# Performance work log

Measured on AMD Instinct MI355X. Metric: run time of the kernel, lower is better.

## Reference

```python
import jax, jax.numpy as jnp
import numpy as np
from jax import lax

B, C, H, W = 32, 256, 64, 64
MCH = 16   # max(8, 256//16)
KS = 5     # ECA 1D kernel: int((log2(256)+1)/2)=4 -> odd-adjust 5
EPS = 1e-5

def setup_inputs() -> dict:
    key = jax.random.key(0)
    ks = jax.random.split(key, 9)
    return {
        "x": jax.random.normal(ks[0], (B, C, H, W), jnp.float32),
        "w10": jax.random.normal(ks[1], (MCH, C), jnp.float32) * 0.05,   # 1x1 conv C->MCH
        "w11": jax.random.normal(ks[2], (C, MCH), jnp.float32) * 0.05,   # 1x1 conv MCH->C
        "bn_gamma": jax.random.normal(ks[3], (MCH,), jnp.float32) * 0.1 + 1.0,
        "bn_beta": jax.random.normal(ks[4], (MCH,), jnp.float32) * 0.1,
        "bn_mean": jax.random.normal(ks[5], (MCH,), jnp.float32) * 0.1,
        "bn_var": jax.random.uniform(ks[6], (MCH,), jnp.float32, 0.5, 1.5),
        "w20": jax.random.normal(ks[7], (KS,), jnp.float32) * 0.2,       # 1D ECA kernel
        "w21": jax.random.normal(ks[8], (1, 1, 3, 3), jnp.float32) * 0.2,  # spatial 3x3
    }

def reference(x, w10, w11, bn_gamma, bn_beta, bn_mean, bn_var, w20, w21):
    b, c, h, w = x.shape
    # --- channel (ECA) branch: global avg pool -> 1D conv over channel dim ---
    pooled = jnp.mean(x, axis=(2, 3))                      # [b, c]
    f_ch = lax.conv_general_dilated(
        pooled[:, None, :], w20[None, None, :], (1,), 'SAME',
        dimension_numbers=('NCH', 'OIH', 'NCH'))[:, 0, :]   # [b, c]
    f_ch = f_ch[:, :, None, None]                           # [b, c, 1, 1] (no sigmoid, as in source)
    # --- spatial branch: channel mean -> 3x3 conv -> sigmoid ---
    f_sa = jax.nn.sigmoid(lax.conv_general_dilated(
        jnp.mean(x, axis=1, keepdims=True), w21, (1, 1), 'SAME',
        dimension_numbers=('NCHW', 'OIHW', 'NCHW')))        # [b, 1, h, w]
    # --- coordinate branch ---
    x_h = jnp.mean(x, axis=3)                               # [b, c, h]
    x_w = jnp.mean(x, axis=2)                               # [b, c, w]
    cat = jnp.concatenate([x_h, x_w], axis=2)               # [b, c, h+w]
    y = jnp.einsum('mc,bcl->bml', w10, cat)                 # 1x1 conv
    inv = lax.rsqrt(bn_var + EPS) * bn_gamma                # BN (inference)
    y = jax.nn.relu(y * inv[None, :, None] + (bn_beta - bn_mean * inv)[None, :, None])
    yh, yw = y[:, :, :h], y[:, :, h:]
    s_h = jax.nn.sigmoid(jnp.einsum('cm,bmh->bch', w11, yh))[:, :, :, None]  # [b,c,h,1]
    s_w = jax.nn.sigmoid(jnp.einsum('cm,bmw->bcw', w11, yw))[:, :, None, :]  # [b,c,1,w]
    F = f_ch + s_h * s_w + f_sa
    return x * F
```

## Files before the change

### kernel.cpp

```cpp
#include <hip/hip_runtime.h>
#include <hip/hip_bf16.h>

#define NB 32
#define NC 256
#define NH 64
#define NW 64

typedef unsigned short u16;

__device__ int   g_mode;
__device__ float g_cmeanp[NB * 16 * 4096];
__device__ float g_catT[NB * 128 * NC];
__device__ float g_fch[NB * NC];
__device__ float g_fsa[NB * 4096];
__device__ float g_sh[NB * NC * 64];
__device__ float g_sw[NB * NC * 64];

__device__ __forceinline__ float bf2f(unsigned int u) {
    union { unsigned int i; float f; } v; v.i = u << 16; return v.f;
}
__device__ __forceinline__ u16 f2bf(float f) {
    union { float f; unsigned int i; } v; v.f = f;
    unsigned int i = v.i;
    unsigned int r = (i + 0x7fffu + ((i >> 16) & 1u)) >> 16;
    return (u16)r;
}
__device__ __forceinline__ unsigned int pack2(float a, float b) {
    return (unsigned int)f2bf(a) | ((unsigned int)f2bf(b) << 16);
}
__device__ __forceinline__ float sigmoidf_(float x) {
    return 1.f / (1.f + expf(-x));
}

__device__ __forceinline__ void loadx8(const void* x, size_t i8, int mode, float* v) {
    if (mode) {
        const uint4 u = ((const uint4*)x)[i8];
        v[0] = bf2f(u.x & 0xffffu); v[1] = bf2f(u.x >> 16);
        v[2] = bf2f(u.y & 0xffffu); v[3] = bf2f(u.y >> 16);
        v[4] = bf2f(u.z & 0xffffu); v[5] = bf2f(u.z >> 16);
        v[6] = bf2f(u.w & 0xffffu); v[7] = bf2f(u.w >> 16);
    } else {
        const float4 a = ((const float4*)x)[i8 * 2];
        const float4 b = ((const float4*)x)[i8 * 2 + 1];
        v[0] = a.x; v[1] = a.y; v[2] = a.z; v[3] = a.w;
        v[4] = b.x; v[5] = b.y; v[6] = b.z; v[7] = b.w;
    }
}
__device__ __forceinline__ float loadw(const void* p, int i, int mode) {
    return mode ? bf2f((unsigned int)((const u16*)p)[i]) : ((const float*)p)[i];
}
__device__ __forceinline__ void store8(void* o, size_t i8, int mode, const float* v) {
    if (mode) {
        uint4 u;
        u.x = pack2(v[0], v[1]);
        u.y = pack2(v[2], v[3]);
        u.z = pack2(v[4], v[5]);
        u.w = pack2(v[6], v[7]);
        ((uint4*)o)[i8] = u;
    } else {
        ((float4*)o)[i8 * 2]     = make_float4(v[0], v[1], v[2], v[3]);
        ((float4*)o)[i8 * 2 + 1] = make_float4(v[4], v[5], v[6], v[7]);
    }
}

__global__ __launch_bounds__(256) void kSniff(const u16* __restrict__ xr) {
    __shared__ int cnt;
    if (threadIdx.x == 0) cnt = 0;
    __syncthreads();
    int local = 0;
#pragma unroll
    for (int i = 0; i < 8; ++i) {
        const u16 w = xr[(threadIdx.x * 8 + i) * 2];
        const unsigned e = (w >> 7) & 0xffu;
        if (w == 0 || (e >= 0x40u && e <= 0x90u)) ++local;
    }
    atomicAdd(&cnt, local);
    __syncthreads();
    if (threadIdx.x == 0) g_mode = (cnt >= 1536) ? 1 : 0;
}

__global__ __launch_bounds__(256) void kA(const void* __restrict__ x) {
    __shared__ unsigned int sliceP[4][2048];
    __shared__ float rowsum[16 * 64];
    __shared__ float colsum[16 * 64];

    const int t  = threadIdx.x;
    const int ln = t & 63, wv = t >> 6;
    const int cg = blockIdx.x;
    const int b  = blockIdx.y;
    const int mode = g_mode;

    float colacc[4][8];
#pragma unroll
    for (int cc = 0; cc < 4; ++cc)
#pragma unroll
        for (int k = 0; k < 8; ++k) colacc[cc][k] = 0.f;

    const int ch0 = cg * 16 + wv * 4;
    const size_t i8base = (((size_t)(b * NC + ch0)) << 9) + ln;

    for (int p = 0; p < 8; ++p) {
        float cme[8];
#pragma unroll
        for (int k = 0; k < 8; ++k) cme[k] = 0.f;
#pragma unroll
        for (int cc = 0; cc < 4; ++cc) {
            float v[8];
            loadx8(x, i8base + (((size_t)cc) << 9) + p * 64, mode, v);
#pragma unroll
            for (int k = 0; k < 8; ++k) {
                cme[k] += v[k];
                colacc[cc][k] += v[k];
            }
            float s = ((v[0] + v[1]) + (v[2] + v[3])) + ((v[4] + v[5]) + (v[6] + v[7]));
            s += __shfl_xor(s, 1);
            s += __shfl_xor(s, 2);
            s += __shfl_xor(s, 4);
            if ((ln & 7) == 0)
                rowsum[(wv * 4 + cc) * 64 + p * 8 + (ln >> 3)] = s;
        }
        uint4 pk;
        pk.x = pack2(cme[0], cme[1]);
        pk.y = pack2(cme[2], cme[3]);
        pk.z = pack2(cme[4], cme[5]);
        pk.w = pack2(cme[6], cme[7]);
        *(uint4*)&sliceP[wv][p * 256 + ln * 4] = pk;
    }

#pragma unroll
    for (int cc = 0; cc < 4; ++cc)
#pragma unroll
        for (int k = 0; k < 8; ++k) {
            float v = colacc[cc][k];
            v += __shfl_xor(v, 8);
            v += __shfl_xor(v, 16);
            v += __shfl_xor(v, 32);
            colacc[cc][k] = v;
        }
    if (ln < 8) {
#pragma unroll
        for (int cc = 0; cc < 4; ++cc) {
            *(float4*)&colsum[(wv * 4 + cc) * 64 + ln * 8] =
                make_float4(colacc[cc][0], colacc[cc][1], colacc[cc][2], colacc[cc][3]);
            *(float4*)&colsum[(wv * 4 + cc) * 64 + ln * 8 + 4] =
                make_float4(colacc[cc][4], colacc[cc][5], colacc[cc][6], colacc[cc][7]);
        }
    }
    __syncthreads();

    const float inv64 = 1.f / 64.f;
    {
        const int lc = t & 15;
#pragma unroll
        for (int r = 0; r < 8; ++r) {
            const int l = r * 16 + (t >> 4);
            const float val =
                (l < 64 ? rowsum[lc * 64 + l] : colsum[lc * 64 + (l - 64)]) * inv64;
            g_catT[((size_t)(b * 128 + l)) * NC + cg * 16 + lc] = val;
        }
    }
    {
        const int u0 = t * 8;
        float acc[16];
#pragma unroll
        for (int k = 0; k < 16; ++k) acc[k] = 0.f;
#pragma unroll
        for (int w = 0; w < 4; ++w) {
            const uint4 qa = *(const uint4*)&sliceP[w][u0];
            const uint4 qb = *(const uint4*)&sliceP[w][u0 + 4];
            const unsigned int uu[8] = {qa.x, qa.y, qa.z, qa.w, qb.x, qb.y, qb.z, qb.w};
#pragma unroll
            for (int k = 0; k < 8; ++k) {
                acc[2 * k]     += bf2f(uu[k] & 0xffffu);
                acc[2 * k + 1] += bf2f(uu[k] >> 16);
            }
        }
        const float invC = 1.f / 256.f;
        float* dst = g_cmeanp + (((size_t)(b * 16 + cg)) << 12) + t * 16;
#pragma unroll
        for (int k4 = 0; k4 < 4; ++k4)
            *(float4*)(dst + k4 * 4) = make_float4(acc[k4 * 4] * invC,
                                                   acc[k4 * 4 + 1] * invC,
                                                   acc[k4 * 4 + 2] * invC,
                                                   acc[k4 * 4 + 3] * invC);
    }
}

__global__ __launch_bounds__(256) void kB(
    const void* __restrict__ w10, const void* __restrict__ w11,
    const void* __restrict__ bn_gamma, const void* __restrict__ bn_beta,
    const void* __restrict__ bn_mean, const void* __restrict__ bn_var,
    const void* __restrict__ w20, const void* __restrict__ w21) {

    __shared__ float w10_lds[16 * 260];
    __shared__ float w11_lds[2048];
    __shared__ float y_lds[16 * 65];
    __shared__ float cm[4096];
    __shared__ float pooled[260];
    __shared__ float bnA[16], bnBv[16];

    const int t  = threadIdx.x;
    const int bx = blockIdx.x;
    const int half = bx >> 1, csplit = bx & 1;
    const int b  = blockIdx.y;
    const int mode = g_mode;

    for (int j = t; j < 4096; j += 256)
        w10_lds[(j >> 8) * 260 + (j & 255)] = loadw(w10, j, mode);
    for (int j = t; j < 2048; j += 256)
        w11_lds[j] = loadw(w11, csplit * 2048 + j, mode);
    if (t < 16) {
        const float inv = rsqrtf(loadw(bn_var, t, mode) + 1e-5f) *
                          loadw(bn_gamma, t, mode);
        bnA[t]  = inv;
        bnBv[t] = loadw(bn_beta, t, mode) - loadw(bn_mean, t, mode) * inv;
    }
    __syncthreads();

    {
        const int m = t & 15, li = t >> 4;
#pragma unroll
        for (int rep = 0; rep < 4; ++rep) {
            const int l = rep * 16 + li;
            const float4* cr =
                (const float4*)(g_catT + ((size_t)(b * 128 + half * 64 + l)) * NC);
            const float4* wr = (const float4*)(w10_lds + m * 260);
            float acc = 0.f;
#pragma unroll 8
            for (int c4 = 0; c4 < 64; ++c4) {
                const float4 a = wr[c4], v = cr[c4];
                acc = fmaf(a.x, v.x, fmaf(a.y, v.y, fmaf(a.z, v.z, fmaf(a.w, v.w, acc))));
            }
            y_lds[m * 65 + l] = fmaxf(fmaf(acc, bnA[m], bnBv[m]), 0.f);
        }
    }
    __syncthreads();

    {
        const int h = t & 63, q = t >> 6;
        float yr[16];
#pragma unroll
        for (int mm = 0; mm < 16; ++mm) yr[mm] = y_lds[mm * 65 + h];
        float* sout = half ? g_sw : g_sh;
        const size_t sb = ((size_t)b) * NC * 64;
        for (int ci = 0; ci < 32; ++ci) {
            const int cl = q * 32 + ci;
            const float4* wrow = (const float4*)(w11_lds + cl * 16);
            const float4 w0 = wrow[0], w1 = wrow[1], w2 = wrow[2], w3 = wrow[3];
            float acc;
            acc = fmaf(w0.x, yr[0], w0.y * yr[1]);
            acc = fmaf(w0.z, yr[2], acc); acc = fmaf(w0.w, yr[3], acc);
            acc = fmaf(w1.x, yr[4], acc); acc = fmaf(w1.y, yr[5], acc);
            acc = fmaf(w1.z, yr[6], acc); acc = fmaf(w1.w, yr[7], acc);
            acc = fmaf(w2.x, yr[8], acc); acc = fmaf(w2.y, yr[9], acc);
            acc = fmaf(w2.z, yr[10], acc); acc = fmaf(w2.w, yr[11], acc);
            acc = fmaf(w3.x, yr[12], acc); acc = fmaf(w3.y, yr[13], acc);
            acc = fmaf(w3.z, yr[14], acc); acc = fmaf(w3.w, yr[15], acc);
            sout[sb + (size_t)(csplit * 128 + cl) * 64 + h] = sigmoidf_(acc);
        }
    }

    if (bx == 0) {
        float p = 0.f;
        for (int l = 0; l < 64; ++l)
            p += g_catT[((size_t)(b * 128 + l)) * NC + t];
        pooled[2 + t] = p * (1.f / 64.f);
        if (t < 2) { pooled[t] = 0.f; pooled[258 + t] = 0.f; }
        __syncthreads();
        float w20f[5];
#pragma unroll
        for (int k = 0; k < 5; ++k) w20f[k] = loadw(w20, k, mode);
        float acc = 0.f;
#pragma unroll
        for (int k = 0; k < 5; ++k) acc = fmaf(w20f[k], pooled[t + k], acc);
        g_fch[b * NC + t] = acc;
    } else if (bx == 1) {
#pragma unroll
        for (int it = 0; it < 4; ++it) {
            const int j = it * 1024 + t * 4;
            float4 s = make_float4(0.f, 0.f, 0.f, 0.f);
            for (int gcg = 0; gcg < 16; ++gcg) {
                const float4 v =
                    *(const float4*)&g_cmeanp[(((size_t)(b * 16 + gcg)) << 12) + j];
                s.x += v.x; s.y += v.y; s.z += v.z; s.w += v.w;
            }
            *(float4*)&cm[j] = s;
        }
        __syncthreads();
        float w21f[9];
#pragma unroll
        for (int k = 0; k < 9; ++k) w21f[k] = loadw(w21, k, mode);
        for (int r = 0; r < 16; ++r) {
            const int j = r * 256 + t;
            const int hh = j >> 6, ww = j & 63;
            float acc = 0.f;
#pragma unroll
            for (int dy = 0; dy < 3; ++dy) {
                const int hy = hh + dy - 1;
                if (hy < 0 || hy > 63) continue;
#pragma unroll
                for (int dx = 0; dx < 3; ++dx) {
                    const int wx = ww + dx - 1;
                    if (wx < 0 || wx > 63) continue;
                    acc = fmaf(w21f[dy * 3 + dx], cm[hy * 64 + wx], acc);
                }
            }
            g_fsa[b * 4096 + j] = sigmoidf_(acc);
        }
    }
}

__global__ __launch_bounds__(256) void kC(const void* __restrict__ x,
                                          void* __restrict__ out) {
    const unsigned e = blockIdx.x * 256 + threadIdx.x;
    const int w0 = (e & 7) << 3;
    const int h  = (e >> 3) & 63;
    const int c  = (e >> 9) & 255;
    const int b  = e >> 17;
    const int mode = g_mode;

    float v[8];
    loadx8(x, e, mode, v);

    const float fc = g_fch[b * NC + c];
    const float sh = g_sh[((size_t)(b * NC + c)) * 64 + h];
    const float* swp = g_sw + ((size_t)(b * NC + c)) * 64 + w0;
    const float* fsp = g_fsa + (size_t)b * 4096 + h * 64 + w0;
    const float4 swa = *(const float4*)(swp);
    const float4 swb = *(const float4*)(swp + 4);
    const float4 fsa = *(const float4*)(fsp);
    const float4 fsb = *(const float4*)(fsp + 4);

    float r[8];
    r[0] = v[0] * (fc + sh * swa.x + fsa.x);
    r[1] = v[1] * (fc + sh * swa.y + fsa.y);
    r[2] = v[2] * (fc + sh * swa.z + fsa.z);
    r[3] = v[3] * (fc + sh * swa.w + fsa.w);
    r[4] = v[4] * (fc + sh * swb.x + fsb.x);
    r[5] = v[5] * (fc + sh * swb.y + fsb.y);
    r[6] = v[6] * (fc + sh * swb.z + fsb.z);
    r[7] = v[7] * (fc + sh * swb.w + fsb.w);

    store8(out, e, mode, r);
}

extern "C" void kernel_launch(void* const* d_in, const int* in_sizes, int n_in,
                              void* d_out, int out_size, void* d_ws, size_t ws_size,
                              hipStream_t stream) {
    const void* x        = d_in[0];
    const void* w10      = d_in[1];
    const void* w11      = d_in[2];
    const void* bn_gamma = d_in[3];
    const void* bn_beta  = d_in[4];
    const void* bn_mean  = d_in[5];
    const void* bn_var   = d_in[6];
    const void* w20      = d_in[7];
    const void* w21      = d_in[8];

    kSniff<<<1, 256, 0, stream>>>((const u16*)x);
    kA<<<dim3(16, NB), 256, 0, stream>>>(x);
    kB<<<dim3(4, NB), 256, 0, stream>>>(w10, w11, bn_gamma, bn_beta,
                                        bn_mean, bn_var, w20, w21);
    kC<<<(NB * NC * NH * NW / 8) / 256, 256, 0, stream>>>(x, d_out);
}
```

Before: 314.5 us.

## Fold sniff into kA, precompute partial 1x1 conv, split spatial conv across blocks

```diff
diff --git a/kernel.cpp b/kernel.cpp
--- a/kernel.cpp
+++ b/kernel.cpp
@@ -10,7 +10,8 @@
 
 __device__ int   g_mode;
 __device__ float g_cmeanp[NB * 16 * 4096];
-__device__ float g_catT[NB * 128 * NC];
+__device__ float g_yp[NB * 16 * 16 * 128];
+__device__ float g_pooled[NB * NC];
 __device__ float g_fch[NB * NC];
 __device__ float g_fsa[NB * 4096];
 __device__ float g_sh[NB * NC * 64];
@@ -63,32 +64,37 @@
     }
 }
 
-__global__ __launch_bounds__(256) void kSniff(const u16* __restrict__ xr) {
-    __shared__ int cnt;
-    if (threadIdx.x == 0) cnt = 0;
-    __syncthreads();
-    int local = 0;
-#pragma unroll
-    for (int i = 0; i < 8; ++i) {
-        const u16 w = xr[(threadIdx.x * 8 + i) * 2];
-        const unsigned e = (w >> 7) & 0xffu;
-        if (w == 0 || (e >= 0x40u && e <= 0x90u)) ++local;
-    }
-    atomicAdd(&cnt, local);
-    __syncthreads();
-    if (threadIdx.x == 0) g_mode = (cnt >= 1536) ? 1 : 0;
-}
-
-__global__ __launch_bounds__(256) void kA(const void* __restrict__ x) {
+__global__ __launch_bounds__(256) void kA(const void* __restrict__ x,
+                                          const void* __restrict__ w10) {
     __shared__ unsigned int sliceP[4][2048];
     __shared__ float rowsum[16 * 64];
     __shared__ float colsum[16 * 64];
+    __shared__ float w10s[256];
+    __shared__ int scnt;
 
     const int t  = threadIdx.x;
     const int ln = t & 63, wv = t >> 6;
     const int cg = blockIdx.x;
     const int b  = blockIdx.y;
-    const int mode = g_mode;
+
+    if (t == 0) scnt = 0;
+    __syncthreads();
+    {
+        const u16* xr = (const u16*)x;
+        int local = 0;
+#pragma unroll
+        for (int i = 0; i < 8; ++i) {
+            const u16 w = xr[(t * 8 + i) * 2];
+            const unsigned e = (w >> 7) & 0xffu;
+            if (w == 0 || (e >= 0x40u && e <= 0x90u)) ++local;
+        }
+        atomicAdd(&scnt, local);
+    }
+    __syncthreads();
+    const int mode = (scnt >= 1536) ? 1 : 0;
+    if ((blockIdx.x | blockIdx.y) == 0 && t == 0) g_mode = mode;
+
+    w10s[t] = loadw(w10, (t >> 4) * NC + cg * 16 + (t & 15), mode);
 
     float colacc[4][8];
 #pragma unroll
@@ -148,17 +154,6 @@
     }
     __syncthreads();
 
-    const float inv64 = 1.f / 64.f;
-    {
-        const int lc = t & 15;
-#pragma unroll
-        for (int r = 0; r < 8; ++r) {
-            const int l = r * 16 + (t >> 4);
-            const float val =
-                (l < 64 ? rowsum[lc * 64 + l] : colsum[lc * 64 + (l - 64)]) * inv64;
-            g_catT[((size_t)(b * 128 + l)) * NC + cg * 16 + lc] = val;
-        }
-    }
     {
         const int u0 = t * 8;
         float acc[16];
@@ -184,18 +179,56 @@
                                                    acc[k4 * 4 + 2] * invC,
                                                    acc[k4 * 4 + 3] * invC);
     }
+
+    {
+        const int lc = t >> 4, j = t & 15;
+        const float* rs = rowsum + lc * 64 + j * 4;
+        float s = (rs[0] + rs[1]) + (rs[2] + rs[3]);
+        s += __shfl_xor(s, 1);
+        s += __shfl_xor(s, 2);
+        s += __shfl_xor(s, 4);
+        s += __shfl_xor(s, 8);
+        if (j == 0) g_pooled[b * NC + cg * 16 + lc] = s * (1.f / 4096.f);
+    }
+
+    {
+        const int m = t >> 4, l0 = (t & 15) * 8;
+        const float* base = (l0 < 64) ? (rowsum + l0) : (colsum + l0 - 64);
+        float acc[8];
+#pragma unroll
+        for (int k = 0; k < 8; ++k) acc[k] = 0.f;
+#pragma unroll
+        for (int lc = 0; lc < 16; ++lc) {
+            const float wvv = w10s[m * 16 + lc];
+            const float4 s0 = *(const float4*)(base + lc * 64);
+            const float4 s1 = *(const float4*)(base + lc * 64 + 4);
+            acc[0] = fmaf(wvv, s0.x, acc[0]);
+            acc[1] = fmaf(wvv, s0.y, acc[1]);
+            acc[2] = fmaf(wvv, s0.z, acc[2]);
+            acc[3] = fmaf(wvv, s0.w, acc[3]);
+            acc[4] = fmaf(wvv, s1.x, acc[4]);
+            acc[5] = fmaf(wvv, s1.y, acc[5]);
+            acc[6] = fmaf(wvv, s1.z, acc[6]);
+            acc[7] = fmaf(wvv, s1.w, acc[7]);
+        }
+        const float inv64 = 1.f / 64.f;
+        float* dst = g_yp + ((((size_t)b * 16 + cg) * 16 + m) << 7) + l0;
+        *(float4*)dst =
+            make_float4(acc[0] * inv64, acc[1] * inv64, acc[2] * inv64, acc[3] * inv64);
+        *(float4*)(dst + 4) =
+            make_float4(acc[4] * inv64, acc[5] * inv64, acc[6] * inv64, acc[7] * inv64);
+    }
 }
 
 __global__ __launch_bounds__(256) void kB(
-    const void* __restrict__ w10, const void* __restrict__ w11,
+    const void* __restrict__ w11,
     const void* __restrict__ bn_gamma, const void* __restrict__ bn_beta,
     const void* __restrict__ bn_mean, const void* __restrict__ bn_var,
     const void* __restrict__ w20, const void* __restrict__ w21) {
 
-    __shared__ float w10_lds[16 * 260];
     __shared__ float w11_lds[2048];
     __shared__ float y_lds[16 * 65];
-    __shared__ float cm[4096];
+    __shared__ float cm[18 * 64];
     __shared__ float pooled[260];
     __shared__ float bnA[16], bnBv[16];
 
@@ -205,8 +238,6 @@
     const int b  = blockIdx.y;
     const int mode = g_mode;
 
-    for (int j = t; j < 4096; j += 256)
-        w10_lds[(j >> 8) * 260 + (j & 255)] = loadw(w10, j, mode);
     for (int j = t; j < 2048; j += 256)
         w11_lds[j] = loadw(w11, csplit * 2048 + j, mode);
     if (t < 16) {
@@ -218,20 +249,17 @@
     __syncthreads();
 
     {
-        const int m = t & 15, li = t >> 4;
-#pragma unroll
-        for (int rep = 0; rep < 4; ++rep) {
-            const int l = rep * 16 + li;
-            const float4* cr =
-                (const float4*)(g_catT + ((size_t)(b * 128 + half * 64 + l)) * NC);
-            const float4* wr = (const float4*)(w10_lds + m * 260);
-            float acc = 0.f;
-#pragma unroll 8
-            for (int c4 = 0; c4 < 64; ++c4) {
-                const float4 a = wr[c4], v = cr[c4];
-                acc = fmaf(a.x, v.x, fmaf(a.y, v.y, fmaf(a.z, v.z, fmaf(a.w, v.w, acc))));
-            }
-            y_lds[m * 65 + l] = fmaxf(fmaf(acc, bnA[m], bnBv[m]), 0.f);
+        const int l = t & 63;
+        const float* src0 = g_yp + ((size_t)b << 15) + half * 64 + l;
+#pragma unroll
+        for (int r = 0; r < 4; ++r) {
+            const int m = r * 4 + (t >> 6);
+            const float* src = src0 + m * 128;
+            float s = 0.f;
+#pragma unroll
+            for (int cgi = 0; cgi < 16; ++cgi)
+                s += src[cgi * 2048];
+            y_lds[m * 65 + l] = fmaxf(fmaf(s, bnA[m], bnBv[m]), 0.f);
         }
     }
     __syncthreads();
@@ -260,11 +288,45 @@
         }
     }
 
+    {
+        const int r0 = bx * 16;
+        const int c0 = (r0 == 0) ? 0 : (r0 - 1);
+        const int c1 = (r0 + 16 > 63) ? 63 : (r0 + 16);
+        const int n  = (c1 - c0 + 1) * 64;
+        const float* srcb = g_cmeanp + (((size_t)b * 16) << 12) + c0 * 64;
+        for (int j = t; j < n; j += 256) {
+            float s = 0.f;
+#pragma unroll
+            for (int gcg = 0; gcg < 16; ++gcg)
+                s += srcb[((size_t)gcg << 12) + j];
+            cm[j] = s;
+        }
+        __syncthreads();
+        float w21f[9];
+#pragma unroll
+        for (int k = 0; k < 9; ++k) w21f[k] = loadw(w21, k, mode);
+#pragma unroll
+        for (int rr = 0; rr < 4; ++rr) {
+            const int j  = rr * 256 + t;
+            const int hh = r0 + (j >> 6), ww = j & 63;
+            float acc = 0.f;
+#pragma unroll
+            for (int dy = 0; dy < 3; ++dy) {
+                const int hy = hh + dy - 1;
+                if (hy < 0 || hy > 63) continue;
+#pragma unroll
+                for (int dx = 0; dx < 3; ++dx) {
+                    const int wx = ww + dx - 1;
+                    if (wx < 0 || wx > 63) continue;
+                    acc = fmaf(w21f[dy * 3 + dx], cm[(hy - c0) * 64 + wx], acc);
+                }
+            }
+            g_fsa[b * 4096 + hh * 64 + ww] = sigmoidf_(acc);
+        }
+    }
+
     if (bx == 0) {
-        float p = 0.f;
-        for (int l = 0; l < 64; ++l)
-            p += g_catT[((size_t)(b * 128 + l)) * NC + t];
-        pooled[2 + t] = p * (1.f / 64.f);
+        pooled[2 + t] = g_pooled[b * NC + t];
         if (t < 2) { pooled[t] = 0.f; pooled[258 + t] = 0.f; }
         __syncthreads();
         float w20f[5];
@@ -274,39 +336,6 @@
 #pragma unroll
         for (int k = 0; k < 5; ++k) acc = fmaf(w20f[k], pooled[t + k], acc);
         g_fch[b * NC + t] = acc;
-    } else if (bx == 1) {
-#pragma unroll
-        for (int it = 0; it < 4; ++it) {
-            const int j = it * 1024 + t * 4;
-            float4 s = make_float4(0.f, 0.f, 0.f, 0.f);
-            for (int gcg = 0; gcg < 16; ++gcg) {
-                const float4 v =
-                    *(const float4*)&g_cmeanp[(((size_t)(b * 16 + gcg)) << 12) + j];
-                s.x += v.x; s.y += v.y; s.z += v.z; s.w += v.w;
-            }
-            *(float4*)&cm[j] = s;
-        }
-        __syncthreads();
-        float w21f[9];
-#pragma unroll
-        for (int k = 0; k < 9; ++k) w21f[k] = loadw(w21, k, mode);
-        for (int r = 0; r < 16; ++r) {
-            const int j = r * 256 + t;
-            const int hh = j >> 6, ww = j & 63;
-            float acc = 0.f;
-#pragma unroll
-            for (int dy = 0; dy < 3; ++dy) {
-                const int hy = hh + dy - 1;
-                if (hy < 0 || hy > 63) continue;
-#pragma unroll
-                for (int dx = 0; dx < 3; ++dx) {
-                    const int wx = ww + dx - 1;
-                    if (wx < 0 || wx > 63) continue;
-                    acc = fmaf(w21f[dy * 3 + dx], cm[hy * 64 + wx], acc);
-                }
-            }
-            g_fsa[b * 4096 + j] = sigmoidf_(acc);
-        }
     }
 }
 
@@ -357,9 +386,8 @@
     const void* w20      = d_in[7];
     const void* w21      = d_in[8];
 
-    kSniff<<<1, 256, 0, stream>>>((const u16*)x);
-    kA<<<dim3(16, NB), 256, 0, stream>>>(x);
-    kB<<<dim3(4, NB), 256, 0, stream>>>(w10, w11, bn_gamma, bn_beta,
+    kA<<<dim3(16, NB), 256, 0, stream>>>(x, w10);
+    kB<<<dim3(4, NB), 256, 0, stream>>>(w11, bn_gamma, bn_beta,
                                         bn_mean, bn_var, w20, w21);
     kC<<<(NB * NC * NH * NW / 8) / 256, 256, 0, stream>>>(x, d_out);
 }
```

After: 290.2 us. -7.7%, faster.
